# Kernel tuning notes

Measured on AMD Instinct MI355X. Metric: run time of the kernel, lower is better.

Reference implementation:

```python
import jax, jax.numpy as jnp
import numpy as np

MAX_LEN = 3

def _attention(h, enc, w1, b1, w2):
    # h: [B,H], enc: [B,S,H]
    B, S, H = enc.shape
    hs = jnp.broadcast_to(h[:, None, :], (B, S, H))
    x = jnp.tanh(jnp.concatenate([enc, hs], axis=-1) @ w1.T + b1)  # [B,S,H]
    e = (x @ w2.T)[..., 0]                                         # [B,S]
    alpha = jax.nn.softmax(e, axis=1)
    return jnp.einsum('bs,bsd->bd', alpha, enc)                    # [B,H]

def _gru_cell(x, h, w_ih, w_hh, b_ih, b_hh):
    # torch GRU gate order: r, z, n
    H = h.shape[-1]
    gi = x @ w_ih.T + b_ih   # [B,3H]
    gh = h @ w_hh.T + b_hh
    i_r, i_z, i_n = gi[:, :H], gi[:, H:2*H], gi[:, 2*H:]
    h_r, h_z, h_n = gh[:, :H], gh[:, H:2*H], gh[:, 2*H:]
    r = jax.nn.sigmoid(i_r + h_r)
    z = jax.nn.sigmoid(i_z + h_z)
    n = jnp.tanh(i_n + r * h_n)
    return (1.0 - z) * n + z * h

def setup_inputs() -> dict:
    key = jax.random.key(0)
    ks = jax.random.split(key, 16)
    B, S, H, DW = 1024, 40, 1024, 512
    V0 = V1 = 4000
    EMB_N = V0 + V1 + 1
    sc = lambda fan: 1.0 / np.sqrt(fan)
    inp = {
        'encoder_outputs': jax.random.normal(ks[0], (B, S, H), jnp.float32),
        'encoder_hidden': jax.random.normal(ks[1], (1, B, H), jnp.float32),
        'targets': jax.random.randint(ks[2], (MAX_LEN, B), 0, V0),
        'emb': jax.random.normal(ks[3], (EMB_N, DW), jnp.float32) * 0.02,
        'attn_w1': jax.random.normal(ks[4], (H, 2 * H), jnp.float32) * sc(2 * H),
        'attn_b1': jnp.zeros((H,), jnp.float32),
        'attn_w2': jax.random.normal(ks[5], (1, H), jnp.float32) * sc(H),
        'w_ih': jax.random.normal(ks[6], (3 * H, H + DW), jnp.float32) * sc(H),
        'w_hh': jax.random.normal(ks[7], (3 * H, H), jnp.float32) * sc(H),
        'b_ih': jnp.zeros((3 * H,), jnp.float32),
        'b_hh': jnp.zeros((3 * H,), jnp.float32),
        'out0_w': jax.random.normal(ks[8], (V0, H), jnp.float32) * sc(H),
        'out0_b': jnp.zeros((V0,), jnp.float32),
        'out1_w': jax.random.normal(ks[9], (V1, H), jnp.float32) * sc(H),
        'out1_b': jnp.zeros((V1,), jnp.float32),
    }
    return inp

def reference(encoder_outputs, encoder_hidden, targets, emb, attn_w1, attn_b1,
              attn_w2, w_ih, w_hh, b_ih, b_hh, out0_w, out0_b, out1_w, out1_b):
    B = encoder_outputs.shape[0]
    h = encoder_hidden[0]  # n_layers=1, unidirectional -> init state passthrough
    logs = []
    for t in range(MAX_LEN):
        context = _attention(h, encoder_outputs, attn_w1, attn_b1, attn_w2)
        if t == 0:
            it = jnp.zeros((B,), jnp.int32)
        elif t == 1:
            it = targets[0] + 1
        else:
            it = targets[t - 1] + 36
        x = jnp.concatenate([emb[it], context], axis=1)  # [B, DW+H]
        h = _gru_cell(x, h, w_ih, w_hh, b_ih, b_hh)
        if t == 0 or t == 2:
            logits = h @ out0_w.T + out0_b
        else:
            logits = h @ out1_w.T + out1_b
        logs.append(jax.nn.log_softmax(logits, axis=1))
    return jnp.stack(logs)  # [MAX_LEN, B, V]
```

## Files before the change

### kernel.cpp

```cpp
#include <hip/hip_runtime.h>
#include <hip/hip_bf16.h>
#include <math.h>

#define B_SZ 1024
#define S_SZ 40
#define H_SZ 1024
#define DW_SZ 512
#define V_SZ 4000
#define XW (DW_SZ + H_SZ)
#define NGL 8192

typedef __bf16 bf16x8 __attribute__((ext_vector_type(8)));
typedef float f32x4 __attribute__((ext_vector_type(4)));

__device__ __forceinline__ float fast_tanh(float x) {
    return 1.0f - 2.0f / (1.0f + __expf(2.0f * x));
}
__device__ __forceinline__ float fast_sigmoid(float x) {
    return 1.0f / (1.0f + __expf(-x));
}
__device__ __forceinline__ float bfraw2f(unsigned short u) {
    return __uint_as_float(((unsigned)u) << 16);
}
__device__ __forceinline__ ushort4 cvt4(float4 v) {
    union { ushort4 u; __hip_bfloat16 h[4]; } o;
    o.h[0] = __float2bfloat16(v.x); o.h[1] = __float2bfloat16(v.y);
    o.h[2] = __float2bfloat16(v.z); o.h[3] = __float2bfloat16(v.w);
    return o.u;
}

#define GLL16(gp, lp)                                                                \
    __builtin_amdgcn_global_load_lds((const __attribute__((address_space(1))) void*)(gp), \
                                     (__attribute__((address_space(3))) void*)(lp), 16, 0, 0)

__global__ __launch_bounds__(256, 2) void gemm_bt_pipe128(
    const __hip_bfloat16* __restrict__ A, int lda,
    const __hip_bfloat16* __restrict__ W, int ldw,
    __hip_bfloat16* __restrict__ C, int ldc,
    int nbx, int K) {
    extern __shared__ char smem[];
    const int tid = threadIdx.x;
    const int lane = tid & 63;
    const int wave = tid >> 6;
    const int wm = wave >> 1, wn = wave & 1;
    const int fr = lane & 15, fq = lane >> 4;

    int bid = blockIdx.x;
    { const int cpx = gridDim.x >> 3; bid = (bid & 7) * cpx + (bid >> 3); }
    const int by = bid / nbx;
    const int bm = by * 128;
    const int bn = (bid - by * nbx) * 256;

    const int r0 = tid >> 2;
    const int s0 = (tid & 3) ^ ((tid >> 3) & 3);
    const __hip_bfloat16* gA0 = A + (size_t)(bm + r0) * lda + s0 * 8;
    const __hip_bfloat16* gA1 = A + (size_t)(bm + r0 + 64) * lda + s0 * 8;
    const __hip_bfloat16* gW0 = W + (size_t)(bn + r0) * ldw + s0 * 8;
    const __hip_bfloat16* gW1 = W + (size_t)(bn + r0 + 64) * ldw + s0 * 8;
    const __hip_bfloat16* gW2 = W + (size_t)(bn + r0 + 128) * ldw + s0 * 8;
    const __hip_bfloat16* gW3 = W + (size_t)(bn + r0 + 192) * ldw + s0 * 8;
    const int dst0 = tid * 16;

    int aoff[4], boff[8];
#pragma unroll
    for (int mi = 0; mi < 4; ++mi) {
        const int row = wm * 64 + mi * 16 + fr;
        aoff[mi] = row * 64 + ((fq ^ ((row >> 1) & 3)) << 4);
    }
#pragma unroll
    for (int ni = 0; ni < 8; ++ni) {
        const int col = wn * 128 + ni * 16 + fr;
        boff[ni] = 8192 + col * 64 + ((fq ^ ((col >> 1) & 3)) << 4);
    }

    const int NT = K >> 5;
    f32x4 acc[4][8] = {};

#define STAGE_T(t)                                                    \
    do {                                                              \
        char* sb = smem + ((t) % 3) * 24576;                          \
        const int kk = (t) << 5;                                      \
        GLL16(gA0 + kk, sb + dst0);                                   \
        GLL16(gA1 + kk, sb + dst0 + 4096);                            \
        GLL16(gW0 + kk, sb + 8192 + dst0);                            \
        GLL16(gW1 + kk, sb + 8192 + dst0 + 4096);                     \
        GLL16(gW2 + kk, sb + 8192 + dst0 + 8192);                     \
        GLL16(gW3 + kk, sb + 8192 + dst0 + 12288);                    \
    } while (0)

    STAGE_T(0);
    STAGE_T(1);
    __builtin_amdgcn_sched_barrier(0);
    asm volatile("s_waitcnt vmcnt(6)" ::: "memory");
    __builtin_amdgcn_s_barrier();
    __builtin_amdgcn_sched_barrier(0);

    for (int t = 0; t < NT; ++t) {
        const char* sb = smem + (t % 3) * 24576;
        bf16x8 af[4], bg[8];
#pragma unroll
        for (int ni = 0; ni < 8; ++ni) bg[ni] = *reinterpret_cast<const bf16x8*>(sb + boff[ni]);
#pragma unroll
        for (int mi = 0; mi < 4; ++mi) af[mi] = *reinterpret_cast<const bf16x8*>(sb + aoff[mi]);

        if (t + 2 < NT) STAGE_T(t + 2);

        __builtin_amdgcn_s_setprio(1);
#pragma unroll
        for (int mi = 0; mi < 4; ++mi)
#pragma unroll
            for (int ni = 0; ni < 8; ++ni)
                acc[mi][ni] = __builtin_amdgcn_mfma_f32_16x16x32_bf16(af[mi], bg[ni], acc[mi][ni], 0, 0, 0);
        __builtin_amdgcn_s_setprio(0);

        if (t != NT - 1) {
            __builtin_amdgcn_sched_barrier(0);
            if (t + 2 < NT) asm volatile("s_waitcnt vmcnt(6)" ::: "memory");
            else            asm volatile("s_waitcnt vmcnt(0)" ::: "memory");
            __builtin_amdgcn_s_barrier();
            __builtin_amdgcn_sched_barrier(0);
        }
    }
#undef STAGE_T

#pragma unroll
    for (int mi = 0; mi < 4; ++mi) {
        const int row0 = bm + wm * 64 + mi * 16 + fq * 4;
#pragma unroll
        for (int ni = 0; ni < 8; ++ni) {
            const int col = bn + wn * 128 + ni * 16 + fr;
#pragma unroll
            for (int r = 0; r < 4; ++r)
                C[(size_t)(row0 + r) * ldc + col] = __float2bfloat16(acc[mi][ni][r]);
        }
    }
}

template <int OB, int SWZ>
__global__ __launch_bounds__(256) void gemm_bt_mfma(
    const __hip_bfloat16* __restrict__ A, int lda,
    const __hip_bfloat16* __restrict__ W, int ldw,
    const float* __restrict__ bias,
    void* __restrict__ Cv, int ldc,
    int nbx, int N, int K) {
    __shared__ __align__(16) __hip_bfloat16 As[128 * 32];
    __shared__ __align__(16) __hip_bfloat16 Ws[128 * 32];
    const int tid = threadIdx.x;
    const int lane = tid & 63;
    const int wave = tid >> 6;

    int bid = blockIdx.x;
    if (SWZ) {
        const int cpx = gridDim.x >> 3;
        bid = (bid & 7) * cpx + (bid >> 3);
    }
    const int by = bid / nbx;
    const int bx = bid - by * nbx;
    const int bm = by * 128;
    const int bn = bx * 128;

    const int r0 = tid >> 2;
    const int kk = (tid & 3) * 8;
    const __hip_bfloat16* gA0 = A + (size_t)(bm + r0) * lda + kk;
    const __hip_bfloat16* gA1 = gA0 + (size_t)64 * lda;
    int wrow0 = bn + r0;      if (wrow0 > N - 1) wrow0 = N - 1;
    int wrow1 = bn + r0 + 64; if (wrow1 > N - 1) wrow1 = N - 1;
    const __hip_bfloat16* gW0 = W + (size_t)wrow0 * ldw + kk;
    const __hip_bfloat16* gW1 = W + (size_t)wrow1 * ldw + kk;
    char* As_c = (char*)As + tid * 16;
    char* Ws_c = (char*)Ws + tid * 16;

    const int wr = wave >> 1, wc = wave & 1;
    const int fr = lane & 15, fq = lane >> 4;
    const __hip_bfloat16* Ard = &As[(wr * 64 + fr) * 32 + fq * 8];
    const __hip_bfloat16* Wrd = &Ws[(wc * 64 + fr) * 32 + fq * 8];

    f32x4 acc[4][4] = {};

    for (int k0 = 0; k0 < K; k0 += 32) {
        __syncthreads();
        GLL16(gA0 + k0, As_c);
        GLL16(gA1 + k0, As_c + 4096);
        GLL16(gW0 + k0, Ws_c);
        GLL16(gW1 + k0, Ws_c + 4096);
        __syncthreads();

        bf16x8 af[4], bg[4];
#pragma unroll
        for (int i = 0; i < 4; ++i) {
            af[i] = *reinterpret_cast<const bf16x8*>(Ard + i * 16 * 32);
            bg[i] = *reinterpret_cast<const bf16x8*>(Wrd + i * 16 * 32);
        }
#pragma unroll
        for (int mi = 0; mi < 4; ++mi)
#pragma unroll
            for (int ni = 0; ni < 4; ++ni)
                acc[mi][ni] = __builtin_amdgcn_mfma_f32_16x16x32_bf16(af[mi], bg[ni], acc[mi][ni], 0, 0, 0);
    }

#pragma unroll
    for (int ni = 0; ni < 4; ++ni) {
        const int col = bn + wc * 64 + ni * 16 + fr;
        if (col >= N) continue;
        const float bb = bias ? bias[col] : 0.0f;
#pragma unroll
        for (int mi = 0; mi < 4; ++mi) {
            const int row0 = bm + wr * 64 + mi * 16 + fq * 4;
#pragma unroll
            for (int r = 0; r < 4; ++r) {
                const float v = acc[mi][ni][r] + bb;
                if (OB)
                    reinterpret_cast<__hip_bfloat16*>(Cv)[(size_t)(row0 + r) * ldc + col] = __float2bfloat16(v);
                else
                    reinterpret_cast<float*>(Cv)[(size_t)(row0 + r) * ldc + col] = v;
            }
        }
    }
}

#define F4_ENC (B_SZ * S_SZ * H_SZ / 4)
#define F4_W1A (H_SZ * H_SZ / 4)
#define F4_W1H (H_SZ * H_SZ / 4)
#define F4_WHH (3 * H_SZ * H_SZ / 4)
#define F4_WIH (3 * H_SZ * XW / 4)
#define F4_O0  (V_SZ * H_SZ / 4)
#define F4_O1  (V_SZ * H_SZ / 4)
#define CE0 (F4_ENC)
#define CE1 (CE0 + F4_W1A)
#define CE2 (CE1 + F4_W1H)
#define CE3 (CE2 + F4_WHH)
#define CE4 (CE3 + F4_WIH)
#define CE5 (CE4 + F4_O0)
#define CE6 (CE5 + F4_O1)
__global__ __launch_bounds__(256) void cast_fast_kernel(
    const float* __restrict__ enc, const float* __restrict__ w1,
    const float* __restrict__ whh, const float* __restrict__ wih,
    const float* __restrict__ o0, const float* __restrict__ o1,
    __hip_bfloat16* __restrict__ enc_bf, __hip_bfloat16* __restrict__ w1a_bf,
    __hip_bfloat16* __restrict__ wall0, __hip_bfloat16* __restrict__ wall1,
    __hip_bfloat16* __restrict__ wih_bf) {
    const int i = blockIdx.x * 256 + threadIdx.x;
    ushort4* wall0_u = reinterpret_cast<ushort4*>(wall0);
    ushort4* wall1_u = reinterpret_cast<ushort4*>(wall1);
    if (i < CE0) {
        const float4 v = reinterpret_cast<const float4*>(enc)[i];
        reinterpret_cast<ushort4*>(enc_bf)[i] = cvt4(v);
    } else if (i < CE1) {
        const int li = i - CE0;
        const int r = li >> 8, c = li & 255;
        const float4 v = reinterpret_cast<const float4*>(w1)[r * 512 + c];
        reinterpret_cast<ushort4*>(w1a_bf)[li] = cvt4(v);
    } else if (i < CE2) {
        const int li = i - CE1;
        const int r = li >> 8, c = li & 255;
        const ushort4 u = cvt4(reinterpret_cast<const float4*>(w1)[r * 512 + 256 + c]);
        wall0_u[li] = u;
        wall1_u[li] = u;
    } else if (i < CE3) {
        const int li = i - CE2;
        const ushort4 u = cvt4(reinterpret_cast<const float4*>(whh)[li]);
        wall0_u[262144 + li] = u;
        wall1_u[262144 + li] = u;
    } else if (i < CE4) {
        const int li = i - CE3;
        reinterpret_cast<ushort4*>(wih_bf)[li] = cvt4(reinterpret_cast<const float4*>(wih)[li]);
    } else if (i < CE5) {
        const int li = i - CE4;
        wall0_u[1048576 + li] = cvt4(reinterpret_cast<const float4*>(o0)[li]);
    } else {
        const int li = i - CE5;
        wall1_u[1048576 + li] = cvt4(reinterpret_cast<const float4*>(o1)[li]);
    }
}

__global__ __launch_bounds__(256) void small_prep_kernel(
    const float* __restrict__ emb, const int* __restrict__ targets,
    __hip_bfloat16* __restrict__ x0, __hip_bfloat16* __restrict__ x1, __hip_bfloat16* __restrict__ x2,
    const float* __restrict__ enc_h, float* __restrict__ h, __hip_bfloat16* __restrict__ h_bf,
    const float* __restrict__ b1, const float* __restrict__ b_hh,
    const float* __restrict__ o0b, const float* __restrict__ o1b,
    float* __restrict__ bias0, float* __restrict__ bias1) {
    const int blk = blockIdx.x;
    const int tid = threadIdx.x;
    if (blk < 3072) {
        if (tid >= 128) return;
        const int t = blk >> 10;
        const int b = blk & 1023;
        int it; __hip_bfloat16* x;
        if (t == 0) { it = 0; x = x0; }
        else if (t == 1) { it = targets[b] + 1; x = x1; }
        else { it = targets[B_SZ + b] + 36; x = x2; }
        float4 v = reinterpret_cast<const float4*>(emb + (size_t)it * DW_SZ)[tid];
        reinterpret_cast<ushort4*>(x + (size_t)b * XW)[tid] = cvt4(v);
    } else if (blk < 4096) {
        const int i = (blk - 3072) * 256 + tid;
        const float4 v = reinterpret_cast<const float4*>(enc_h)[i];
        reinterpret_cast<float4*>(h)[i] = v;
        reinterpret_cast<ushort4*>(h_bf)[i] = cvt4(v);
    } else {
        float* bt = (blk == 4096) ? bias0 : bias1;
        const float* ob = (blk == 4096) ? o0b : o1b;
        for (int j = tid; j < NGL; j += 256) {
            float v;
            if (j < H_SZ) v = b1[j];
            else if (j < 4 * H_SZ) v = b_hh[j - H_SZ];
            else if (j < 4 * H_SZ + V_SZ) v = ob[j - 4 * H_SZ];
            else v = 0.0f;
            bt[j] = v;
        }
    }
}

__global__ __launch_bounds__(256) void attn_ls_kernel(
    const __hip_bfloat16* __restrict__ enc,
    const __hip_bfloat16* __restrict__ enc_proj,
    const __hip_bfloat16* __restrict__ hgl,
    const float* __restrict__ w2,
    __hip_bfloat16* __restrict__ x,
    float* __restrict__ outp,
    int nattn) {
    const int blk = blockIdx.x;
    const int tid = threadIdx.x;
    const int lane = tid & 63, wave = tid >> 6;
    __shared__ float s_e[S_SZ];
    __shared__ float s_red[4];
    __shared__ float s_bc;

    if (blk < nattn) {
        const int b = blk;
        float hp[16], wv[16];
        const unsigned short* hgrow = reinterpret_cast<const unsigned short*>(hgl) + (size_t)b * NGL;
#pragma unroll
        for (int p = 0; p < 4; ++p) {
            const int base = p * 256 + lane * 4;
            ushort4 hu = *reinterpret_cast<const ushort4*>(hgrow + base);
            float4 wq = *reinterpret_cast<const float4*>(w2 + base);
            hp[p * 4 + 0] = bfraw2f(hu.x); hp[p * 4 + 1] = bfraw2f(hu.y);
            hp[p * 4 + 2] = bfraw2f(hu.z); hp[p * 4 + 3] = bfraw2f(hu.w);
            wv[p * 4 + 0] = wq.x; wv[p * 4 + 1] = wq.y;
            wv[p * 4 + 2] = wq.z; wv[p * 4 + 3] = wq.w;
        }

        const unsigned short* ep0 = reinterpret_cast<const unsigned short*>(enc_proj) + (size_t)b * S_SZ * H_SZ;
#pragma unroll 2
        for (int i = 0; i < 10; ++i) {
            const int s = wave + 4 * i;
            const unsigned short* row = ep0 + (size_t)s * H_SZ;
            float acc = 0.f;
#pragma unroll
            for (int p = 0; p < 4; ++p) {
                ushort4 eu = *reinterpret_cast<const ushort4*>(row + p * 256 + lane * 4);
                acc += fast_tanh(bfraw2f(eu.x) + hp[p * 4 + 0]) * wv[p * 4 + 0]
                     + fast_tanh(bfraw2f(eu.y) + hp[p * 4 + 1]) * wv[p * 4 + 1]
                     + fast_tanh(bfraw2f(eu.z) + hp[p * 4 + 2]) * wv[p * 4 + 2]
                     + fast_tanh(bfraw2f(eu.w) + hp[p * 4 + 3]) * wv[p * 4 + 3];
            }
#pragma unroll
            for (int off = 32; off > 0; off >>= 1) acc += __shfl_down(acc, off);
            if (lane == 0) s_e[s] = acc;
        }
        __syncthreads();

        float m = -1e30f;
        for (int s = 0; s < S_SZ; ++s) m = fmaxf(m, s_e[s]);
        float sum = 0.f;
        for (int s = 0; s < S_SZ; ++s) sum += __expf(s_e[s] - m);
        const float inv = 1.0f / sum;

        const ushort4* enc_b = reinterpret_cast<const ushort4*>(enc + (size_t)b * S_SZ * H_SZ);
        float4 acc = make_float4(0.f, 0.f, 0.f, 0.f);
        for (int s = 0; s < S_SZ; ++s) {
            const float a = __expf(s_e[s] - m) * inv;
            ushort4 ev = enc_b[s * 256 + tid];
            acc.x += a * bfraw2f(ev.x); acc.y += a * bfraw2f(ev.y);
            acc.z += a * bfraw2f(ev.z); acc.w += a * bfraw2f(ev.w);
        }
        reinterpret_cast<ushort4*>(x + (size_t)b * XW + DW_SZ)[tid] = cvt4(acc);
    } else {
        const int b = blk - nattn;
        const ushort4* row4 = reinterpret_cast<const ushort4*>(
            reinterpret_cast<const unsigned short*>(hgl) + (size_t)b * NGL + 4096);
        float* orow = outp + (size_t)b * V_SZ;

        float m = -1e30f;
        for (int k = tid; k < V_SZ / 4; k += 256) {
            ushort4 u = row4[k];
            m = fmaxf(m, fmaxf(fmaxf(bfraw2f(u.x), bfraw2f(u.y)), fmaxf(bfraw2f(u.z), bfraw2f(u.w))));
        }
#pragma unroll
        for (int off = 32; off > 0; off >>= 1) m = fmaxf(m, __shfl_down(m, off));
        if (lane == 0) s_red[wave] = m;
        __syncthreads();
        if (tid == 0) s_bc = fmaxf(fmaxf(s_red[0], s_red[1]), fmaxf(s_red[2], s_red[3]));
        __syncthreads();
        m = s_bc;

        float sum = 0.f;
        for (int k = tid; k < V_SZ / 4; k += 256) {
            ushort4 u = row4[k];
            sum += expf(bfraw2f(u.x) - m) + expf(bfraw2f(u.y) - m)
                 + expf(bfraw2f(u.z) - m) + expf(bfraw2f(u.w) - m);
        }
#pragma unroll
        for (int off = 32; off > 0; off >>= 1) sum += __shfl_down(sum, off);
        __syncthreads();
        if (lane == 0) s_red[wave] = sum;
        __syncthreads();
        if (tid == 0) s_bc = logf(s_red[0] + s_red[1] + s_red[2] + s_red[3]) + m;
        __syncthreads();
        const float ls = s_bc;

        for (int k = tid; k < V_SZ / 4; k += 256) {
            ushort4 u = row4[k];
            float4 o = make_float4(bfraw2f(u.x) - ls, bfraw2f(u.y) - ls,
                                   bfraw2f(u.z) - ls, bfraw2f(u.w) - ls);
            reinterpret_cast<float4*>(orow)[k] = o;
        }
    }
}

__global__ __launch_bounds__(256) void gru_gate_kernel(
    const __hip_bfloat16* __restrict__ gi,
    const __hip_bfloat16* __restrict__ hgl,
    float* __restrict__ h,
    __hip_bfloat16* __restrict__ h_bf) {
    const int idx = blockIdx.x * 256 + threadIdx.x;
    const int b = idx >> 10;
    const int j = idx & 1023;
    const unsigned short* gib = reinterpret_cast<const unsigned short*>(gi) + (size_t)b * 3 * H_SZ;
    const unsigned short* ghb = reinterpret_cast<const unsigned short*>(hgl) + (size_t)b * NGL + H_SZ;
    const float i_r = bfraw2f(gib[j]), i_z = bfraw2f(gib[H_SZ + j]), i_n = bfraw2f(gib[2 * H_SZ + j]);
    const float h_r = bfraw2f(ghb[j]), h_z = bfraw2f(ghb[H_SZ + j]), h_n = bfraw2f(ghb[2 * H_SZ + j]);
    const float r = fast_sigmoid(i_r + h_r);
    const float z = fast_sigmoid(i_z + h_z);
    const float n = fast_tanh(i_n + r * h_n);
    const float hv = (1.0f - z) * n + z * h[idx];
    h[idx] = hv;
    h_bf[idx] = __float2bfloat16(hv);
}

extern "C" void kernel_launch(void* const* d_in, const int* in_sizes, int n_in,
                              void* d_out, int out_size, void* d_ws, size_t ws_size,
                              hipStream_t stream) {
    const float* enc    = (const float*)d_in[0];
    const float* enc_h  = (const float*)d_in[1];
    const int*   tgt    = (const int*)d_in[2];
    const float* emb    = (const float*)d_in[3];
    const float* w1     = (const float*)d_in[4];
    const float* b1     = (const float*)d_in[5];
    const float* w2     = (const float*)d_in[6];
    const float* w_ih   = (const float*)d_in[7];
    const float* w_hh   = (const float*)d_in[8];
    const float* b_ih   = (const float*)d_in[9];
    const float* b_hh   = (const float*)d_in[10];
    const float* out0_w = (const float*)d_in[11];
    const float* out0_b = (const float*)d_in[12];
    const float* out1_w = (const float*)d_in[13];
    const float* out1_b = (const float*)d_in[14];
    float* out = (float*)d_out;

    char* wp = (char*)d_ws;
    auto carve = [&](size_t bytes) { char* p = wp; wp += (bytes + 255) & ~(size_t)255; return p; };
    __hip_bfloat16* enc_bf  = (__hip_bfloat16*)carve((size_t)B_SZ * S_SZ * H_SZ * 2);
    __hip_bfloat16* encp_bf = (__hip_bfloat16*)carve((size_t)B_SZ * S_SZ * H_SZ * 2);
    __hip_bfloat16* w1a_bf  = (__hip_bfloat16*)carve((size_t)H_SZ * H_SZ * 2);
    __hip_bfloat16* wall0   = (__hip_bfloat16*)carve((size_t)NGL * H_SZ * 2);
    __hip_bfloat16* wall1   = (__hip_bfloat16*)carve((size_t)NGL * H_SZ * 2);
    __hip_bfloat16* wih_bf  = (__hip_bfloat16*)carve((size_t)3 * H_SZ * XW * 2);
    float*          bias0   = (float*)carve((size_t)NGL * 4);
    float*          bias1   = (float*)carve((size_t)NGL * 4);
    float*          h       = (float*)carve((size_t)B_SZ * H_SZ * 4);
    __hip_bfloat16* h_bf    = (__hip_bfloat16*)carve((size_t)B_SZ * H_SZ * 2);
    __hip_bfloat16* hgl     = (__hip_bfloat16*)carve((size_t)B_SZ * NGL * 2);
    __hip_bfloat16* x_bf[3];
    for (int t = 0; t < 3; ++t) x_bf[t] = (__hip_bfloat16*)carve((size_t)B_SZ * XW * 2);
    __hip_bfloat16* gi_bf   = (__hip_bfloat16*)carve((size_t)B_SZ * 3 * H_SZ * 2);

    cast_fast_kernel<<<CE6 / 256, 256, 0, stream>>>(enc, w1, w_hh, w_ih, out0_w, out1_w,
                                                    enc_bf, w1a_bf, wall0, wall1, wih_bf);
    hipMemsetAsync(wall0 + (size_t)(4 * H_SZ + V_SZ) * H_SZ, 0, (size_t)96 * H_SZ * 2, stream);
    hipMemsetAsync(wall1 + (size_t)(4 * H_SZ + V_SZ) * H_SZ, 0, (size_t)96 * H_SZ * 2, stream);
    small_prep_kernel<<<4098, 256, 0, stream>>>(emb, tgt, x_bf[0], x_bf[1], x_bf[2],
                                                enc_h, h, h_bf, b1, b_hh, out0_b, out1_b,
                                                bias0, bias1);

    gemm_bt_pipe128<<<(B_SZ * S_SZ / 128) * (H_SZ / 256), 256, 3 * 24576, stream>>>(
        enc_bf, H_SZ, w1a_bf, H_SZ, encp_bf, H_SZ, H_SZ / 256, H_SZ);

    gemm_bt_mfma<1, 0><<<(B_SZ / 128) * 32, 256, 0, stream>>>(
        h_bf, H_SZ, wall0, H_SZ, bias0, hgl, NGL, 32, 4 * H_SZ, H_SZ);

    attn_ls_kernel<<<B_SZ, 256, 0, stream>>>(enc_bf, encp_bf, hgl, w2, x_bf[0], out, B_SZ);

    for (int t = 0; t < 3; ++t) {
        gemm_bt_mfma<1, 0><<<(B_SZ / 128) * 24, 256, 0, stream>>>(
            x_bf[t], XW, wih_bf, XW, b_ih, gi_bf, 3 * H_SZ, 24, 3 * H_SZ, XW);

        gru_gate_kernel<<<(B_SZ * H_SZ) / 256, 256, 0, stream>>>(gi_bf, hgl, h, h_bf);

        if (t == 0) {
            gemm_bt_mfma<1, 0><<<(B_SZ / 128) * 64, 256, 0, stream>>>(
                h_bf, H_SZ, wall0, H_SZ, bias0, hgl, NGL, 64, NGL, H_SZ);
        } else if (t == 1) {
            gemm_bt_mfma<1, 0><<<(B_SZ / 128) * 64, 256, 0, stream>>>(
                h_bf, H_SZ, wall1, H_SZ, bias1, hgl, NGL, 64, NGL, H_SZ);
        } else {
            gemm_bt_mfma<1, 0><<<(B_SZ / 128) * 32, 256, 0, stream>>>(
                h_bf, H_SZ, wall0 + (size_t)4 * H_SZ * H_SZ, H_SZ, bias0 + 4 * H_SZ,
                hgl + 4 * H_SZ, NGL, 32, 4 * H_SZ, H_SZ);
        }

        float* outp = out + (size_t)t * B_SZ * V_SZ;
        if (t < 2) {
            attn_ls_kernel<<<2 * B_SZ, 256, 0, stream>>>(enc_bf, encp_bf, hgl, w2, x_bf[t + 1],
                                                         outp, B_SZ);
        } else {
            attn_ls_kernel<<<B_SZ, 256, 0, stream>>>(enc_bf, encp_bf, hgl, w2, x_bf[0],
                                                     outp, 0);
        }
    }
}
```

Measured before the change: 546.0 us.

## Enlarge encoder projection GEMM to 256x256 tiles with 512 threads and K=64 stages

The encoder-projection GEMM moves from a 128x256 tile with 256 threads and a triple-buffered K=32 pipeline to a 256x256 tile with 512 threads and a double-buffered K=64 pipeline. It uses 128KB of LDS with an 8-way XOR swizzle and splits each stage into two MFMA halves, issuing the next stage's loads between them. The aim is more operand reuse per byte loaded and fewer barriers per unit of K. Separately, the cast kernel now has each thread convert four float4 chunks, which cuts the block count by four. The trade-offs are one block per CU with heavy LDS use and less latency hiding, plus a grid of 640 blocks that may fill the CUs unevenly.

```diff
diff --git a/kernel.cpp b/kernel.cpp
--- a/kernel.cpp
+++ b/kernel.cpp
@@ -33,7 +33,7 @@
     __builtin_amdgcn_global_load_lds((const __attribute__((address_space(1))) void*)(gp), \
                                      (__attribute__((address_space(3))) void*)(lp), 16, 0, 0)
 
-__global__ __launch_bounds__(256, 2) void gemm_bt_pipe128(
+__global__ __launch_bounds__(512, 1) void gemm_bt_pipe256(
     const __hip_bfloat16* __restrict__ A, int lda,
     const __hip_bfloat16* __restrict__ W, int ldw,
     __hip_bfloat16* __restrict__ C, int ldc,
@@ -42,93 +42,107 @@
     const int tid = threadIdx.x;
     const int lane = tid & 63;
     const int wave = tid >> 6;
-    const int wm = wave >> 1, wn = wave & 1;
+    const int wm = wave >> 2, wn = wave & 3;
     const int fr = lane & 15, fq = lane >> 4;
 
     int bid = blockIdx.x;
     { const int cpx = gridDim.x >> 3; bid = (bid & 7) * cpx + (bid >> 3); }
     const int by = bid / nbx;
-    const int bm = by * 128;
+    const int bm = by * 256;
     const int bn = (bid - by * nbx) * 256;
 
-    const int r0 = tid >> 2;
-    const int s0 = (tid & 3) ^ ((tid >> 3) & 3);
-    const __hip_bfloat16* gA0 = A + (size_t)(bm + r0) * lda + s0 * 8;
-    const __hip_bfloat16* gA1 = A + (size_t)(bm + r0 + 64) * lda + s0 * 8;
-    const __hip_bfloat16* gW0 = W + (size_t)(bn + r0) * ldw + s0 * 8;
-    const __hip_bfloat16* gW1 = W + (size_t)(bn + r0 + 64) * ldw + s0 * 8;
-    const __hip_bfloat16* gW2 = W + (size_t)(bn + r0 + 128) * ldw + s0 * 8;
-    const __hip_bfloat16* gW3 = W + (size_t)(bn + r0 + 192) * ldw + s0 * 8;
+    const int r0 = tid >> 3;
+    const int sl = ((tid & 7) ^ (r0 & 7)) * 8;
+    const __hip_bfloat16* gA = A + (size_t)(bm + r0) * lda + sl;
+    const __hip_bfloat16* gW = W + (size_t)(bn + r0) * ldw + sl;
     const int dst0 = tid * 16;
 
-    int aoff[4], boff[8];
-#pragma unroll
-    for (int mi = 0; mi < 4; ++mi) {
-        const int row = wm * 64 + mi * 16 + fr;
-        aoff[mi] = row * 64 + ((fq ^ ((row >> 1) & 3)) << 4);
-    }
-#pragma unroll
-    for (int ni = 0; ni < 8; ++ni) {
-        const int col = wn * 128 + ni * 16 + fr;
-        boff[ni] = 8192 + col * 64 + ((fq ^ ((col >> 1) & 3)) << 4);
-    }
-
-    const int NT = K >> 5;
-    f32x4 acc[4][8] = {};
-
-#define STAGE_T(t)                                                    \
-    do {                                                              \
-        char* sb = smem + ((t) % 3) * 24576;                          \
-        const int kk = (t) << 5;                                      \
-        GLL16(gA0 + kk, sb + dst0);                                   \
-        GLL16(gA1 + kk, sb + dst0 + 4096);                            \
-        GLL16(gW0 + kk, sb + 8192 + dst0);                            \
-        GLL16(gW1 + kk, sb + 8192 + dst0 + 4096);                     \
-        GLL16(gW2 + kk, sb + 8192 + dst0 + 8192);                     \
-        GLL16(gW3 + kk, sb + 8192 + dst0 + 12288);                    \
+    int aoff[8], boff[4];
+#pragma unroll
+    for (int mi = 0; mi < 8; ++mi) {
+        const int row = wm * 128 + mi * 16 + fr;
+        aoff[mi] = row * 128 + ((fq ^ (row & 7)) << 4);
+    }
+#pragma unroll
+    for (int ni = 0; ni < 4; ++ni) {
+        const int row = wn * 64 + ni * 16 + fr;
+        boff[ni] = 32768 + row * 128 + ((fq ^ (row & 7)) << 4);
+    }
+
+    const int NT = K >> 6;
+    f32x4 acc[8][4] = {};
+
+#define STAGE256(t)                                                       \
+    do {                                                                  \
+        char* sb = smem + ((t) & 1) * 65536;                              \
+        const int kk = (t) << 6;                                          \
+        GLL16(gA + kk, sb + dst0);                                        \
+        GLL16(gA + (size_t)64 * lda + kk, sb + dst0 + 8192);              \
+        GLL16(gA + (size_t)128 * lda + kk, sb + dst0 + 16384);            \
+        GLL16(gA + (size_t)192 * lda + kk, sb + dst0 + 24576);            \
+        GLL16(gW + kk, sb + 32768 + dst0);                                \
+        GLL16(gW + (size_t)64 * ldw + kk, sb + 32768 + dst0 + 8192);      \
+        GLL16(gW + (size_t)128 * ldw + kk, sb + 32768 + dst0 + 16384);    \
+        GLL16(gW + (size_t)192 * ldw + kk, sb + 32768 + dst0 + 24576);    \
     } while (0)
 
-    STAGE_T(0);
-    STAGE_T(1);
+    STAGE256(0);
+    STAGE256(1);
     __builtin_amdgcn_sched_barrier(0);
-    asm volatile("s_waitcnt vmcnt(6)" ::: "memory");
+    asm volatile("s_waitcnt vmcnt(8)" ::: "memory");
     __builtin_amdgcn_s_barrier();
     __builtin_amdgcn_sched_barrier(0);
 
     for (int t = 0; t < NT; ++t) {
-        const char* sb = smem + (t % 3) * 24576;
-        bf16x8 af[4], bg[8];
-#pragma unroll
-        for (int ni = 0; ni < 8; ++ni) bg[ni] = *reinterpret_cast<const bf16x8*>(sb + boff[ni]);
-#pragma unroll
-        for (int mi = 0; mi < 4; ++mi) af[mi] = *reinterpret_cast<const bf16x8*>(sb + aoff[mi]);
-
-        if (t + 2 < NT) STAGE_T(t + 2);
-
+        const char* sb = smem + (t & 1) * 65536;
+        bf16x8 af[8], bg[4];
+
+#pragma unroll
+        for (int ni = 0; ni < 4; ++ni) bg[ni] = *reinterpret_cast<const bf16x8*>(sb + boff[ni]);
+#pragma unroll
+        for (int mi = 0; mi < 8; ++mi) af[mi] = *reinterpret_cast<const bf16x8*>(sb + aoff[mi]);
         __builtin_amdgcn_s_setprio(1);
 #pragma unroll
-        for (int mi = 0; mi < 4; ++mi)
-#pragma unroll
-            for (int ni = 0; ni < 8; ++ni)
+        for (int mi = 0; mi < 8; ++mi)
+#pragma unroll
+            for (int ni = 0; ni < 4; ++ni)
                 acc[mi][ni] = __builtin_amdgcn_mfma_f32_16x16x32_bf16(af[mi], bg[ni], acc[mi][ni], 0, 0, 0);
         __builtin_amdgcn_s_setprio(0);
 
+#pragma unroll
+        for (int ni = 0; ni < 4; ++ni) bg[ni] = *reinterpret_cast<const bf16x8*>(sb + (boff[ni] ^ 64));
+#pragma unroll
+        for (int mi = 0; mi < 8; ++mi) af[mi] = *reinterpret_cast<const bf16x8*>(sb + (aoff[mi] ^ 64));
+        __builtin_amdgcn_sched_barrier(0);
+        asm volatile("s_waitcnt lgkmcnt(0)" ::: "memory");
+        __builtin_amdgcn_s_barrier();
+        __builtin_amdgcn_sched_barrier(0);
+        if (t + 2 < NT) STAGE256(t + 2);
+
+        __builtin_amdgcn_s_setprio(1);
+#pragma unroll
+        for (int mi = 0; mi < 8; ++mi)
+#pragma unroll
+            for (int ni = 0; ni < 4; ++ni)
+                acc[mi][ni] = __builtin_amdgcn_mfma_f32_16x16x32_bf16(af[mi], bg[ni], acc[mi][ni], 0, 0, 0);
+        __builtin_amdgcn_s_setprio(0);
+
         if (t != NT - 1) {
             __builtin_amdgcn_sched_barrier(0);
-            if (t + 2 < NT) asm volatile("s_waitcnt vmcnt(6)" ::: "memory");
+            if (t + 2 < NT) asm volatile("s_waitcnt vmcnt(8)" ::: "memory");
             else            asm volatile("s_waitcnt vmcnt(0)" ::: "memory");
             __builtin_amdgcn_s_barrier();
             __builtin_amdgcn_sched_barrier(0);
         }
     }
-#undef STAGE_T
-
-#pragma unroll
-    for (int mi = 0; mi < 4; ++mi) {
-        const int row0 = bm + wm * 64 + mi * 16 + fq * 4;
-#pragma unroll
-        for (int ni = 0; ni < 8; ++ni) {
-            const int col = bn + wn * 128 + ni * 16 + fr;
+#undef STAGE256
+
+#pragma unroll
+    for (int mi = 0; mi < 8; ++mi) {
+        const int row0 = bm + wm * 128 + mi * 16 + fq * 4;
+#pragma unroll
+        for (int ni = 0; ni < 4; ++ni) {
+            const int col = bn + wn * 64 + ni * 16 + fr;
 #pragma unroll
             for (int r = 0; r < 4; ++r)
                 C[(size_t)(row0 + r) * ldc + col] = __float2bfloat16(acc[mi][ni][r]);
@@ -239,37 +253,39 @@
     __hip_bfloat16* __restrict__ enc_bf, __hip_bfloat16* __restrict__ w1a_bf,
     __hip_bfloat16* __restrict__ wall0, __hip_bfloat16* __restrict__ wall1,
     __hip_bfloat16* __restrict__ wih_bf) {
-    const int i = blockIdx.x * 256 + threadIdx.x;
     ushort4* wall0_u = reinterpret_cast<ushort4*>(wall0);
     ushort4* wall1_u = reinterpret_cast<ushort4*>(wall1);
-    if (i < CE0) {
-        const float4 v = reinterpret_cast<const float4*>(enc)[i];
-        reinterpret_cast<ushort4*>(enc_bf)[i] = cvt4(v);
-    } else if (i < CE1) {
-        const int li = i - CE0;
-        const int r = li >> 8, c = li & 255;
-        const float4 v = reinterpret_cast<const float4*>(w1)[r * 512 + c];
-        reinterpret_cast<ushort4*>(w1a_bf)[li] = cvt4(v);
-    } else if (i < CE2) {
-        const int li = i - CE1;
-        const int r = li >> 8, c = li & 255;
-        const ushort4 u = cvt4(reinterpret_cast<const float4*>(w1)[r * 512 + 256 + c]);
-        wall0_u[li] = u;
-        wall1_u[li] = u;
-    } else if (i < CE3) {
-        const int li = i - CE2;
-        const ushort4 u = cvt4(reinterpret_cast<const float4*>(whh)[li]);
-        wall0_u[262144 + li] = u;
-        wall1_u[262144 + li] = u;
-    } else if (i < CE4) {
-        const int li = i - CE3;
-        reinterpret_cast<ushort4*>(wih_bf)[li] = cvt4(reinterpret_cast<const float4*>(wih)[li]);
-    } else if (i < CE5) {
-        const int li = i - CE4;
-        wall0_u[1048576 + li] = cvt4(reinterpret_cast<const float4*>(o0)[li]);
-    } else {
-        const int li = i - CE5;
-        wall1_u[1048576 + li] = cvt4(reinterpret_cast<const float4*>(o1)[li]);
+    const int base = blockIdx.x * 1024 + threadIdx.x;
+#pragma unroll
+    for (int k = 0; k < 4; ++k) {
+        const int i = base + k * 256;
+        if (i < CE0) {
+            reinterpret_cast<ushort4*>(enc_bf)[i] = cvt4(reinterpret_cast<const float4*>(enc)[i]);
+        } else if (i < CE1) {
+            const int li = i - CE0;
+            const int r = li >> 8, c = li & 255;
+            reinterpret_cast<ushort4*>(w1a_bf)[li] = cvt4(reinterpret_cast<const float4*>(w1)[r * 512 + c]);
+        } else if (i < CE2) {
+            const int li = i - CE1;
+            const int r = li >> 8, c = li & 255;
+            const ushort4 u = cvt4(reinterpret_cast<const float4*>(w1)[r * 512 + 256 + c]);
+            wall0_u[li] = u;
+            wall1_u[li] = u;
+        } else if (i < CE3) {
+            const int li = i - CE2;
+            const ushort4 u = cvt4(reinterpret_cast<const float4*>(whh)[li]);
+            wall0_u[262144 + li] = u;
+            wall1_u[262144 + li] = u;
+        } else if (i < CE4) {
+            const int li = i - CE3;
+            reinterpret_cast<ushort4*>(wih_bf)[li] = cvt4(reinterpret_cast<const float4*>(wih)[li]);
+        } else if (i < CE5) {
+            const int li = i - CE4;
+            wall0_u[1048576 + li] = cvt4(reinterpret_cast<const float4*>(o0)[li]);
+        } else {
+            const int li = i - CE5;
+            wall1_u[1048576 + li] = cvt4(reinterpret_cast<const float4*>(o1)[li]);
+        }
     }
 }
 
@@ -476,15 +492,15 @@
     for (int t = 0; t < 3; ++t) x_bf[t] = (__hip_bfloat16*)carve((size_t)B_SZ * XW * 2);
     __hip_bfloat16* gi_bf   = (__hip_bfloat16*)carve((size_t)B_SZ * 3 * H_SZ * 2);
 
-    cast_fast_kernel<<<CE6 / 256, 256, 0, stream>>>(enc, w1, w_hh, w_ih, out0_w, out1_w,
-                                                    enc_bf, w1a_bf, wall0, wall1, wih_bf);
+    cast_fast_kernel<<<CE6 / 1024, 256, 0, stream>>>(enc, w1, w_hh, w_ih, out0_w, out1_w,
+                                                     enc_bf, w1a_bf, wall0, wall1, wih_bf);
     hipMemsetAsync(wall0 + (size_t)(4 * H_SZ + V_SZ) * H_SZ, 0, (size_t)96 * H_SZ * 2, stream);
     hipMemsetAsync(wall1 + (size_t)(4 * H_SZ + V_SZ) * H_SZ, 0, (size_t)96 * H_SZ * 2, stream);
     small_prep_kernel<<<4098, 256, 0, stream>>>(emb, tgt, x_bf[0], x_bf[1], x_bf[2],
                                                 enc_h, h, h_bf, b1, b_hh, out0_b, out1_b,
                                                 bias0, bias1);
 
-    gemm_bt_pipe128<<<(B_SZ * S_SZ / 128) * (H_SZ / 256), 256, 3 * 24576, stream>>>(
+    gemm_bt_pipe256<<<(B_SZ * S_SZ / 256) * (H_SZ / 256), 512, 2 * 65536, stream>>>(
         enc_bf, H_SZ, w1a_bf, H_SZ, encp_bf, H_SZ, H_SZ / 256, H_SZ);
 
     gemm_bt_mfma<1, 0><<<(B_SZ / 128) * 32, 256, 0, stream>>>(
```

Result: slower. 560.1 us (+2.6%).

## Precompute embedding part of GRU input GEMM for all steps in one batched GEMM

Applied to the files above, without the earlier changes.

Splits the GRU input projection into an embedding part (K=512) and a context part (K=1024). The embedding part for all three timesteps is computed up front in one larger GEMM over the three contiguous x buffers. Each step's GEMM then only covers the context columns and adds the precomputed partial sums in its epilogue. This shortens the serial per-step GEMM at the cost of an extra workspace buffer, an extra bf16 read, and rounding the partial sum to bf16. The cast kernel is also changed so each thread converts four elements, using a quarter of the blocks.

```diff
diff --git a/kernel.cpp b/kernel.cpp
--- a/kernel.cpp
+++ b/kernel.cpp
@@ -141,6 +141,7 @@
     const __hip_bfloat16* __restrict__ A, int lda,
     const __hip_bfloat16* __restrict__ W, int ldw,
     const float* __restrict__ bias,
+    const __hip_bfloat16* __restrict__ Cin, int ldcin,
     void* __restrict__ Cv, int ldc,
     int nbx, int N, int K) {
     __shared__ __align__(16) __hip_bfloat16 As[128 * 32];
@@ -208,7 +209,9 @@
             const int row0 = bm + wr * 64 + mi * 16 + fq * 4;
 #pragma unroll
             for (int r = 0; r < 4; ++r) {
-                const float v = acc[mi][ni][r] + bb;
+                float v = acc[mi][ni][r] + bb;
+                if (Cin)
+                    v += bfraw2f(reinterpret_cast<const unsigned short*>(Cin)[(size_t)(row0 + r) * ldcin + col]);
                 if (OB)
                     reinterpret_cast<__hip_bfloat16*>(Cv)[(size_t)(row0 + r) * ldc + col] = __float2bfloat16(v);
                 else
@@ -239,37 +242,39 @@
     __hip_bfloat16* __restrict__ enc_bf, __hip_bfloat16* __restrict__ w1a_bf,
     __hip_bfloat16* __restrict__ wall0, __hip_bfloat16* __restrict__ wall1,
     __hip_bfloat16* __restrict__ wih_bf) {
-    const int i = blockIdx.x * 256 + threadIdx.x;
     ushort4* wall0_u = reinterpret_cast<ushort4*>(wall0);
     ushort4* wall1_u = reinterpret_cast<ushort4*>(wall1);
-    if (i < CE0) {
-        const float4 v = reinterpret_cast<const float4*>(enc)[i];
-        reinterpret_cast<ushort4*>(enc_bf)[i] = cvt4(v);
-    } else if (i < CE1) {
-        const int li = i - CE0;
-        const int r = li >> 8, c = li & 255;
-        const float4 v = reinterpret_cast<const float4*>(w1)[r * 512 + c];
-        reinterpret_cast<ushort4*>(w1a_bf)[li] = cvt4(v);
-    } else if (i < CE2) {
-        const int li = i - CE1;
-        const int r = li >> 8, c = li & 255;
-        const ushort4 u = cvt4(reinterpret_cast<const float4*>(w1)[r * 512 + 256 + c]);
-        wall0_u[li] = u;
-        wall1_u[li] = u;
-    } else if (i < CE3) {
-        const int li = i - CE2;
-        const ushort4 u = cvt4(reinterpret_cast<const float4*>(whh)[li]);
-        wall0_u[262144 + li] = u;
-        wall1_u[262144 + li] = u;
-    } else if (i < CE4) {
-        const int li = i - CE3;
-        reinterpret_cast<ushort4*>(wih_bf)[li] = cvt4(reinterpret_cast<const float4*>(wih)[li]);
-    } else if (i < CE5) {
-        const int li = i - CE4;
-        wall0_u[1048576 + li] = cvt4(reinterpret_cast<const float4*>(o0)[li]);
-    } else {
-        const int li = i - CE5;
-        wall1_u[1048576 + li] = cvt4(reinterpret_cast<const float4*>(o1)[li]);
+    const int base = blockIdx.x * 1024 + threadIdx.x;
+#pragma unroll
+    for (int k = 0; k < 4; ++k) {
+        const int i = base + k * 256;
+        if (i < CE0) {
+            reinterpret_cast<ushort4*>(enc_bf)[i] = cvt4(reinterpret_cast<const float4*>(enc)[i]);
+        } else if (i < CE1) {
+            const int li = i - CE0;
+            const int r = li >> 8, c = li & 255;
+            reinterpret_cast<ushort4*>(w1a_bf)[li] = cvt4(reinterpret_cast<const float4*>(w1)[r * 512 + c]);
+        } else if (i < CE2) {
+            const int li = i - CE1;
+            const int r = li >> 8, c = li & 255;
+            const ushort4 u = cvt4(reinterpret_cast<const float4*>(w1)[r * 512 + 256 + c]);
+            wall0_u[li] = u;
+            wall1_u[li] = u;
+        } else if (i < CE3) {
+            const int li = i - CE2;
+            const ushort4 u = cvt4(reinterpret_cast<const float4*>(whh)[li]);
+            wall0_u[262144 + li] = u;
+            wall1_u[262144 + li] = u;
+        } else if (i < CE4) {
+            const int li = i - CE3;
+            reinterpret_cast<ushort4*>(wih_bf)[li] = cvt4(reinterpret_cast<const float4*>(wih)[li]);
+        } else if (i < CE5) {
+            const int li = i - CE4;
+            wall0_u[1048576 + li] = cvt4(reinterpret_cast<const float4*>(o0)[li]);
+        } else {
+            const int li = i - CE5;
+            wall1_u[1048576 + li] = cvt4(reinterpret_cast<const float4*>(o1)[li]);
+        }
     }
 }
 
@@ -476,37 +481,54 @@
     for (int t = 0; t < 3; ++t) x_bf[t] = (__hip_bfloat16*)carve((size_t)B_SZ * XW * 2);
     __hip_bfloat16* gi_bf   = (__hip_bfloat16*)carve((size_t)B_SZ * 3 * H_SZ * 2);
 
-    cast_fast_kernel<<<CE6 / 256, 256, 0, stream>>>(enc, w1, w_hh, w_ih, out0_w, out1_w,
-                                                    enc_bf, w1a_bf, wall0, wall1, wih_bf);
+    const size_t gie_bytes = (size_t)3 * B_SZ * 3 * H_SZ * 2;
+    __hip_bfloat16* gie = nullptr;
+    if ((size_t)(wp - (char*)d_ws) + gie_bytes + 256 <= ws_size)
+        gie = (__hip_bfloat16*)carve(gie_bytes);
+
+    cast_fast_kernel<<<CE6 / 1024, 256, 0, stream>>>(enc, w1, w_hh, w_ih, out0_w, out1_w,
+                                                     enc_bf, w1a_bf, wall0, wall1, wih_bf);
     hipMemsetAsync(wall0 + (size_t)(4 * H_SZ + V_SZ) * H_SZ, 0, (size_t)96 * H_SZ * 2, stream);
     hipMemsetAsync(wall1 + (size_t)(4 * H_SZ + V_SZ) * H_SZ, 0, (size_t)96 * H_SZ * 2, stream);
     small_prep_kernel<<<4098, 256, 0, stream>>>(emb, tgt, x_bf[0], x_bf[1], x_bf[2],
                                                 enc_h, h, h_bf, b1, b_hh, out0_b, out1_b,
                                                 bias0, bias1);
 
+    if (gie) {
+        gemm_bt_mfma<1, 0><<<(3 * B_SZ / 128) * 24, 256, 0, stream>>>(
+            x_bf[0], XW, wih_bf, XW, nullptr, nullptr, 0, gie, 3 * H_SZ, 24, 3 * H_SZ, DW_SZ);
+    }
+
     gemm_bt_pipe128<<<(B_SZ * S_SZ / 128) * (H_SZ / 256), 256, 3 * 24576, stream>>>(
         enc_bf, H_SZ, w1a_bf, H_SZ, encp_bf, H_SZ, H_SZ / 256, H_SZ);
 
     gemm_bt_mfma<1, 0><<<(B_SZ / 128) * 32, 256, 0, stream>>>(
-        h_bf, H_SZ, wall0, H_SZ, bias0, hgl, NGL, 32, 4 * H_SZ, H_SZ);
+        h_bf, H_SZ, wall0, H_SZ, bias0, nullptr, 0, hgl, NGL, 32, 4 * H_SZ, H_SZ);
 
     attn_ls_kernel<<<B_SZ, 256, 0, stream>>>(enc_bf, encp_bf, hgl, w2, x_bf[0], out, B_SZ);
 
     for (int t = 0; t < 3; ++t) {
-        gemm_bt_mfma<1, 0><<<(B_SZ / 128) * 24, 256, 0, stream>>>(
-            x_bf[t], XW, wih_bf, XW, b_ih, gi_bf, 3 * H_SZ, 24, 3 * H_SZ, XW);
+        if (gie) {
+            gemm_bt_mfma<1, 0><<<(B_SZ / 128) * 24, 256, 0, stream>>>(
+                x_bf[t] + DW_SZ, XW, wih_bf + DW_SZ, XW, b_ih,
+                gie + (size_t)t * B_SZ * 3 * H_SZ, 3 * H_SZ,
+                gi_bf, 3 * H_SZ, 24, 3 * H_SZ, H_SZ);
+        } else {
+            gemm_bt_mfma<1, 0><<<(B_SZ / 128) * 24, 256, 0, stream>>>(
+                x_bf[t], XW, wih_bf, XW, b_ih, nullptr, 0, gi_bf, 3 * H_SZ, 24, 3 * H_SZ, XW);
+        }
 
         gru_gate_kernel<<<(B_SZ * H_SZ) / 256, 256, 0, stream>>>(gi_bf, hgl, h, h_bf);
 
         if (t == 0) {
             gemm_bt_mfma<1, 0><<<(B_SZ / 128) * 64, 256, 0, stream>>>(
-                h_bf, H_SZ, wall0, H_SZ, bias0, hgl, NGL, 64, NGL, H_SZ);
+                h_bf, H_SZ, wall0, H_SZ, bias0, nullptr, 0, hgl, NGL, 64, NGL, H_SZ);
         } else if (t == 1) {
             gemm_bt_mfma<1, 0><<<(B_SZ / 128) * 64, 256, 0, stream>>>(
-                h_bf, H_SZ, wall1, H_SZ, bias1, hgl, NGL, 64, NGL, H_SZ);
+                h_bf, H_SZ, wall1, H_SZ, bias1, nullptr, 0, hgl, NGL, 64, NGL, H_SZ);
         } else {
             gemm_bt_mfma<1, 0><<<(B_SZ / 128) * 32, 256, 0, stream>>>(
-                h_bf, H_SZ, wall0 + (size_t)4 * H_SZ * H_SZ, H_SZ, bias0 + 4 * H_SZ,
+                h_bf, H_SZ, wall0 + (size_t)4 * H_SZ * H_SZ, H_SZ, bias0 + 4 * H_SZ, nullptr, 0,
                 hgl + 4 * H_SZ, NGL, 32, 4 * H_SZ, H_SZ);
         }
 
```

Measured after the change: 584.0 us. +7.0%, slower.
